# Kernel tuning notes

Measured on AMD Instinct MI355X. Metric: run time of the kernel, lower is better.

The kernel has to match this reference:

```python
import jax, jax.numpy as jnp
import numpy as np

B, T, C, H = 2, 2048, 2048, 16
HD = C // H  # head_dim = 128


def setup_inputs() -> dict:
    key = jax.random.key(0)
    k1, k2, k3 = jax.random.split(key, 3)
    x = jax.random.normal(k1, (B, T, C), dtype=jnp.float32)
    # causal mask: positions with mask==0 are blocked (masked_fill(mask==0, -inf))
    mask = jnp.tril(jnp.ones((T, T), dtype=bool))[None, None]  # [1,1,T,T]
    W_qkv = jax.random.normal(k2, (C, 3 * C), dtype=jnp.float32) * (C ** -0.5)
    W_proj = jax.random.normal(k3, (C, C), dtype=jnp.float32) * (C ** -0.5)
    b_proj = jnp.zeros((C,), dtype=jnp.float32)
    return {"x": x, "mask": mask, "W_qkv": W_qkv, "W_proj": W_proj, "b_proj": b_proj}


def reference(x, mask, W_qkv, W_proj, b_proj):
    # QKV projection (Linear, bias=False)
    qkv = jnp.einsum('btc,cd->btd', x, W_qkv)            # [B,T,3C]
    qkv = qkv.reshape(B, T, 3, H, HD)
    q = qkv[:, :, 0].transpose(0, 2, 1, 3)               # [B,H,T,HD]
    k = qkv[:, :, 1].transpose(0, 2, 1, 3)
    v = qkv[:, :, 2].transpose(0, 2, 1, 3)
    # scaled dot-product attention (dropout is identity in eval)
    att = jnp.einsum('bhqd,bhkd->bhqk', q, k) / jnp.sqrt(jnp.float32(HD))
    att = jnp.where(mask, att, -jnp.inf)
    att = jax.nn.softmax(att, axis=-1)
    y = jnp.einsum('bhqk,bhkd->bhqd', att, v)            # [B,H,T,HD]
    y = y.transpose(0, 2, 1, 3).reshape(B, T, C)
    return jnp.einsum('btc,cd->btd', y, W_proj) + b_proj
```

## Files before the change

### kernel.cpp

```cpp
#include <hip/hip_runtime.h>
#include <hip/hip_bf16.h>

#define B_  2
#define T_  2048
#define C_  2048
#define H_  16
#define HD_ 128

using bf16x8 = __attribute__((ext_vector_type(8))) __bf16;
using f32x4  = __attribute__((ext_vector_type(4))) float;

__device__ __forceinline__ unsigned short f2bs(float f) {
    __hip_bfloat16 h = __float2bfloat16(f);
    return __builtin_bit_cast(unsigned short, h);
}

__device__ __forceinline__ void gload_lds16(const unsigned short* g, unsigned short* l) {
    __builtin_amdgcn_global_load_lds(
        (const __attribute__((address_space(1))) unsigned int*)g,
        (__attribute__((address_space(3))) unsigned int*)l, 16, 0, 0);
}

__global__ __launch_bounds__(256) void k_prep(const float* __restrict__ x,
                                              unsigned short* __restrict__ XB,
                                              const float* __restrict__ Wqkv,
                                              unsigned short* __restrict__ WQKVT,
                                              const float* __restrict__ Wproj,
                                              unsigned short* __restrict__ WPROJT) {
    __shared__ unsigned short t[64][65];
    int blk = blockIdx.x;
    int tid = threadIdx.x;
    if (blk < 8192) {
        int i = blk * 256 + tid;
        float4 v = reinterpret_cast<const float4*>(x)[i];
        ushort4 o;
        o.x = f2bs(v.x); o.y = f2bs(v.y); o.z = f2bs(v.z); o.w = f2bs(v.w);
        reinterpret_cast<ushort4*>(XB)[i] = o;
        return;
    }
    const float* in;
    unsigned short* out;
    int K = 2048, N, bx, by;
    if (blk < 11264) {
        in = Wqkv; out = WQKVT; N = 6144;
        bx = (blk - 8192) % 96; by = (blk - 8192) / 96;
    } else {
        in = Wproj; out = WPROJT; N = 2048;
        bx = (blk - 11264) % 32; by = (blk - 11264) / 32;
    }
    int k0 = by * 64, n0 = bx * 64;
#pragma unroll
    for (int p = 0; p < 4; ++p) {
        int idx = p * 256 + tid;
        int r = idx >> 4, c = (idx & 15) << 2;
        float4 v = *reinterpret_cast<const float4*>(in + (long)(k0 + r) * N + n0 + c);
        t[r][c] = f2bs(v.x); t[r][c + 1] = f2bs(v.y);
        t[r][c + 2] = f2bs(v.z); t[r][c + 3] = f2bs(v.w);
    }
    __syncthreads();
#pragma unroll
    for (int p = 0; p < 4; ++p) {
        int idx = p * 256 + tid;
        int r = idx >> 4, c = (idx & 15) << 2;
        ushort4 o;
        o.x = t[c][r]; o.y = t[c + 1][r]; o.z = t[c + 2][r]; o.w = t[c + 3][r];
        *reinterpret_cast<ushort4*>(out + (long)(n0 + r) * K + k0 + c) = o;
    }
}

template <int MODE>
__global__ __launch_bounds__(256, 2) void k_gemm(const unsigned short* __restrict__ A,
                                                 const unsigned short* __restrict__ Bt,
                                                 int M, int N, int K,
                                                 unsigned short* __restrict__ qkv,
                                                 float* __restrict__ out,
                                                 const float* __restrict__ bias) {
    __shared__ __align__(16) unsigned short lA[2][128 * 32];
    __shared__ __align__(16) unsigned short lB[2][128 * 32];

    int tid = threadIdx.x;
    int wave = tid >> 6, lane = tid & 63;
    int quad = lane >> 4, l16 = lane & 15;
    int wr = (wave >> 1) * 64, wc = (wave & 1) * 64;
    int m0 = blockIdx.y * 128, n0 = blockIdx.x * 128;

    int lrow = lane >> 2;
    int lcol = (lane & 3) << 3;
    const unsigned short* gA0 = A + (long)(m0 + wave * 32 + lrow) * K + lcol;
    const unsigned short* gA1 = A + (long)(m0 + wave * 32 + 16 + lrow) * K + lcol;
    const unsigned short* gB0 = Bt + (long)(n0 + wave * 32 + lrow) * K + lcol;
    const unsigned short* gB1 = Bt + (long)(n0 + wave * 32 + 16 + lrow) * K + lcol;
    int lofs0 = wave * 1024, lofs1 = wave * 1024 + 512;

    f32x4 zero = {0.f, 0.f, 0.f, 0.f};
    f32x4 acc[4][4];
#pragma unroll
    for (int i = 0; i < 4; ++i)
#pragma unroll
        for (int j = 0; j < 4; ++j) acc[i][j] = zero;

    for (int k0 = 0; k0 < K; k0 += 64) {
        __syncthreads();
#pragma unroll
        for (int h = 0; h < 2; ++h) {
            int kk = k0 + h * 32;
            gload_lds16(gA0 + kk, &lA[h][lofs0]);
            gload_lds16(gA1 + kk, &lA[h][lofs1]);
            gload_lds16(gB0 + kk, &lB[h][lofs0]);
            gload_lds16(gB1 + kk, &lB[h][lofs1]);
        }
        __syncthreads();
#pragma unroll
        for (int h = 0; h < 2; ++h) {
            bf16x8 af[4], bfr[4];
#pragma unroll
            for (int i = 0; i < 4; ++i)
                af[i] = *reinterpret_cast<const bf16x8*>(&lA[h][(wr + i * 16 + l16) * 32 + quad * 8]);
#pragma unroll
            for (int j = 0; j < 4; ++j)
                bfr[j] = *reinterpret_cast<const bf16x8*>(&lB[h][(wc + j * 16 + l16) * 32 + quad * 8]);
#pragma unroll
            for (int i = 0; i < 4; ++i)
#pragma unroll
                for (int j = 0; j < 4; ++j)
                    acc[i][j] = __builtin_amdgcn_mfma_f32_16x16x32_bf16(af[i], bfr[j], acc[i][j], 0, 0, 0);
        }
    }

#pragma unroll
    for (int i = 0; i < 4; ++i) {
#pragma unroll
        for (int j = 0; j < 4; ++j) {
#pragma unroll
            for (int r = 0; r < 4; ++r) {
                int m = m0 + wr + i * 16 + quad * 4 + r;
                int n = n0 + wc + j * 16 + l16;
                float v = acc[i][j][r];
                if (MODE == 0) {
                    int s = n >> 11, col = n & 2047;
                    int h = col >> 7, hd = col & 127;
                    int b = m >> 11, t = m & 2047;
                    long base = (long)s * (B_ * H_ * T_ * HD_);
                    if (s == 2)
                        qkv[base + ((long)(b * H_ + h) * HD_ + hd) * T_ + t] = f2bs(v);
                    else
                        qkv[base + ((long)(b * H_ + h) * T_ + t) * HD_ + hd] = f2bs(v);
                } else {
                    out[(long)m * N + n] = v + bias[n];
                }
            }
        }
    }
}

__global__ __launch_bounds__(256, 2) void k_attn(const unsigned short* __restrict__ qkv,
                                                 unsigned short* __restrict__ y) {
    __shared__ __align__(16) unsigned short lK[64 * 136];
    __shared__ __align__(16) unsigned short lVt[128 * 72];
    __shared__ __align__(16) unsigned short lP[4][2][16 * 72];

    int tid = threadIdx.x;
    int wave = tid >> 6, lane = tid & 63;
    int quad = lane >> 4, l16 = lane & 15;
    int bh = blockIdx.x;
    int ty = (int)blockIdx.y;
    int tile = (ty < 8) ? (15 - ty) : (ty - 8);
    int qb = tile * 128;

    const unsigned short* Qh = qkv + (long)bh * (T_ * HD_);
    const unsigned short* Kh = qkv + (long)(B_ * H_) * T_ * HD_ + (long)bh * (T_ * HD_);
    const unsigned short* Vt = qkv + 2L * (B_ * H_) * T_ * HD_ + (long)bh * (HD_ * T_);

    bf16x8 aQ0[4], aQ1[4];
    const int q0_abs = qb + wave * 32 + l16;
    const int q1_abs = q0_abs + 16;
#pragma unroll
    for (int kk = 0; kk < 4; ++kk) {
        aQ0[kk] = *reinterpret_cast<const bf16x8*>(Qh + (long)q0_abs * HD_ + kk * 32 + quad * 8);
        aQ1[kk] = *reinterpret_cast<const bf16x8*>(Qh + (long)q1_abs * HD_ + kk * 32 + quad * 8);
    }

    const int kR0 = tid >> 4, kC = (tid & 15) << 3;
    const int vR0 = tid >> 3, vC = (tid & 7) << 3;

    int4 kr0, kr1, kr2, kr3, vr0, vr1, vr2, vr3;
    {
        long ko = 0;
        kr0 = *reinterpret_cast<const int4*>(Kh + (ko + kR0)      * HD_ + kC);
        kr1 = *reinterpret_cast<const int4*>(Kh + (ko + kR0 + 16) * HD_ + kC);
        kr2 = *reinterpret_cast<const int4*>(Kh + (ko + kR0 + 32) * HD_ + kC);
        kr3 = *reinterpret_cast<const int4*>(Kh + (ko + kR0 + 48) * HD_ + kC);
        vr0 = *reinterpret_cast<const int4*>(Vt + (long)(vR0)      * T_ + ko + vC);
        vr1 = *reinterpret_cast<const int4*>(Vt + (long)(vR0 + 32) * T_ + ko + vC);
        vr2 = *reinterpret_cast<const int4*>(Vt + (long)(vR0 + 64) * T_ + ko + vC);
        vr3 = *reinterpret_cast<const int4*>(Vt + (long)(vR0 + 96) * T_ + ko + vC);
    }

    float m0_ = -1e30f, l0_ = 0.f, m1_ = -1e30f, l1_ = 0.f;
    f32x4 O0[8], O1[8];
    f32x4 zero = {0.f, 0.f, 0.f, 0.f};
#pragma unroll
    for (int h = 0; h < 8; ++h) { O0[h] = zero; O1[h] = zero; }

    const float scl = 0.08838834764831845f;
    const int kbend = qb + 128;
    const int qmaxw = qb + wave * 32 + 31;

    for (int kb = 0; kb < kbend; kb += 64) {
        __syncthreads();

        *reinterpret_cast<int4*>(&lK[(kR0)      * 136 + kC]) = kr0;
        *reinterpret_cast<int4*>(&lK[(kR0 + 16) * 136 + kC]) = kr1;
        *reinterpret_cast<int4*>(&lK[(kR0 + 32) * 136 + kC]) = kr2;
        *reinterpret_cast<int4*>(&lK[(kR0 + 48) * 136 + kC]) = kr3;
        *reinterpret_cast<int4*>(&lVt[(vR0)      * 72 + vC]) = vr0;
        *reinterpret_cast<int4*>(&lVt[(vR0 + 32) * 72 + vC]) = vr1;
        *reinterpret_cast<int4*>(&lVt[(vR0 + 64) * 72 + vC]) = vr2;
        *reinterpret_cast<int4*>(&lVt[(vR0 + 96) * 72 + vC]) = vr3;

        __syncthreads();

        {
            int nkb = kb + 64;
            long ko = (nkb < kbend) ? nkb : 0;
            kr0 = *reinterpret_cast<const int4*>(Kh + (ko + kR0)      * HD_ + kC);
            kr1 = *reinterpret_cast<const int4*>(Kh + (ko + kR0 + 16) * HD_ + kC);
            kr2 = *reinterpret_cast<const int4*>(Kh + (ko + kR0 + 32) * HD_ + kC);
            kr3 = *reinterpret_cast<const int4*>(Kh + (ko + kR0 + 48) * HD_ + kC);
            vr0 = *reinterpret_cast<const int4*>(Vt + (long)(vR0)      * T_ + ko + vC);
            vr1 = *reinterpret_cast<const int4*>(Vt + (long)(vR0 + 32) * T_ + ko + vC);
            vr2 = *reinterpret_cast<const int4*>(Vt + (long)(vR0 + 64) * T_ + ko + vC);
            vr3 = *reinterpret_cast<const int4*>(Vt + (long)(vR0 + 96) * T_ + ko + vC);
        }

        if (kb > qmaxw) continue;

        f32x4 s0[4], s1[4];
#pragma unroll
        for (int st = 0; st < 4; ++st) { s0[st] = zero; s1[st] = zero; }
#pragma unroll
        for (int kk = 0; kk < 4; ++kk) {
#pragma unroll
            for (int st = 0; st < 4; ++st) {
                bf16x8 kf = *reinterpret_cast<const bf16x8*>(
                    &lK[(st * 16 + l16) * 136 + kk * 32 + quad * 8]);
                s0[st] = __builtin_amdgcn_mfma_f32_16x16x32_bf16(kf, aQ0[kk], s0[st], 0, 0, 0);
                s1[st] = __builtin_amdgcn_mfma_f32_16x16x32_bf16(kf, aQ1[kk], s1[st], 0, 0, 0);
            }
        }

        {
            float xv[4][4];
            float mx = -1e30f;
#pragma unroll
            for (int st = 0; st < 4; ++st)
#pragma unroll
                for (int r = 0; r < 4; ++r) {
                    int key = kb + st * 16 + quad * 4 + r;
                    float v = (key <= q0_abs) ? s0[st][r] * scl : -1e30f;
                    xv[st][r] = v;
                    mx = fmaxf(mx, v);
                }
            mx = fmaxf(mx, __shfl_xor(mx, 16));
            mx = fmaxf(mx, __shfl_xor(mx, 32));
            float mn = fmaxf(m0_, mx);
            float al = __expf(m0_ - mn);
            float rs = 0.f;
#pragma unroll
            for (int st = 0; st < 4; ++st)
#pragma unroll
                for (int r = 0; r < 4; ++r) {
                    float e = __expf(xv[st][r] - mn);
                    xv[st][r] = e;
                    rs += e;
                }
            rs += __shfl_xor(rs, 16);
            rs += __shfl_xor(rs, 32);
            m0_ = mn;
            l0_ = l0_ * al + rs;
#pragma unroll
            for (int st = 0; st < 4; ++st) {
                ushort4 pk;
                pk.x = f2bs(xv[st][0]); pk.y = f2bs(xv[st][1]);
                pk.z = f2bs(xv[st][2]); pk.w = f2bs(xv[st][3]);
                *reinterpret_cast<ushort4*>(&lP[wave][0][l16 * 72 + st * 16 + quad * 4]) = pk;
            }
            float alr[4];
#pragma unroll
            for (int r = 0; r < 4; ++r) alr[r] = __shfl(al, quad * 4 + r);
#pragma unroll
            for (int h = 0; h < 8; ++h)
#pragma unroll
                for (int r = 0; r < 4; ++r) O0[h][r] *= alr[r];
        }
        {
            float xv[4][4];
            float mx = -1e30f;
#pragma unroll
            for (int st = 0; st < 4; ++st)
#pragma unroll
                for (int r = 0; r < 4; ++r) {
                    int key = kb + st * 16 + quad * 4 + r;
                    float v = (key <= q1_abs) ? s1[st][r] * scl : -1e30f;
                    xv[st][r] = v;
                    mx = fmaxf(mx, v);
                }
            mx = fmaxf(mx, __shfl_xor(mx, 16));
            mx = fmaxf(mx, __shfl_xor(mx, 32));
            float mn = fmaxf(m1_, mx);
            float al = __expf(m1_ - mn);
            float rs = 0.f;
#pragma unroll
            for (int st = 0; st < 4; ++st)
#pragma unroll
                for (int r = 0; r < 4; ++r) {
                    float e = __expf(xv[st][r] - mn);
                    xv[st][r] = e;
                    rs += e;
                }
            rs += __shfl_xor(rs, 16);
            rs += __shfl_xor(rs, 32);
            m1_ = mn;
            l1_ = l1_ * al + rs;
#pragma unroll
            for (int st = 0; st < 4; ++st) {
                ushort4 pk;
                pk.x = f2bs(xv[st][0]); pk.y = f2bs(xv[st][1]);
                pk.z = f2bs(xv[st][2]); pk.w = f2bs(xv[st][3]);
                *reinterpret_cast<ushort4*>(&lP[wave][1][l16 * 72 + st * 16 + quad * 4]) = pk;
            }
            float alr[4];
#pragma unroll
            for (int r = 0; r < 4; ++r) alr[r] = __shfl(al, quad * 4 + r);
#pragma unroll
            for (int h = 0; h < 8; ++h)
#pragma unroll
                for (int r = 0; r < 4; ++r) O1[h][r] *= alr[r];
        }

#pragma unroll
        for (int kc = 0; kc < 2; ++kc) {
            bf16x8 pf0 = *reinterpret_cast<const bf16x8*>(
                &lP[wave][0][l16 * 72 + kc * 32 + quad * 8]);
            bf16x8 pf1 = *reinterpret_cast<const bf16x8*>(
                &lP[wave][1][l16 * 72 + kc * 32 + quad * 8]);
#pragma unroll
            for (int h = 0; h < 8; ++h) {
                bf16x8 vf = *reinterpret_cast<const bf16x8*>(
                    &lVt[(h * 16 + l16) * 72 + kc * 32 + quad * 8]);
                O0[h] = __builtin_amdgcn_mfma_f32_16x16x32_bf16(pf0, vf, O0[h], 0, 0, 0);
                O1[h] = __builtin_amdgcn_mfma_f32_16x16x32_bf16(pf1, vf, O1[h], 0, 0, 0);
            }
        }
    }

    int b = bh >> 4, hh = bh & 15;
#pragma unroll
    for (int r = 0; r < 4; ++r) {
        int t0 = qb + wave * 32 + quad * 4 + r;
        float inv0 = 1.f / __shfl(l0_, quad * 4 + r);
#pragma unroll
        for (int h = 0; h < 8; ++h)
            y[(long)(b * T_ + t0) * C_ + hh * HD_ + h * 16 + l16] = f2bs(O0[h][r] * inv0);
        int t1 = t0 + 16;
        float inv1 = 1.f / __shfl(l1_, quad * 4 + r);
#pragma unroll
        for (int h = 0; h < 8; ++h)
            y[(long)(b * T_ + t1) * C_ + hh * HD_ + h * 16 + l16] = f2bs(O1[h][r] * inv1);
    }
}

extern "C" void kernel_launch(void* const* d_in, const int* in_sizes, int n_in,
                              void* d_out, int out_size, void* d_ws, size_t ws_size,
                              hipStream_t stream) {
    const float* x     = (const float*)d_in[0];
    const float* Wqkv  = (const float*)d_in[2];
    const float* Wproj = (const float*)d_in[3];
    const float* bproj = (const float*)d_in[4];
    float* out = (float*)d_out;

    unsigned short* XB     = (unsigned short*)d_ws;
    unsigned short* WQKVT  = XB + 8388608;
    unsigned short* WPROJT = WQKVT + 12582912;
    unsigned short* QKV    = WPROJT + 4194304;
    if (ws_size < 100663296) return;

    k_prep<<<12288, 256, 0, stream>>>(x, XB, Wqkv, WQKVT, Wproj, WPROJT);
    k_gemm<0><<<dim3(6144 / 128, 4096 / 128), 256, 0, stream>>>(XB, WQKVT, 4096, 6144, 2048,
                                                                QKV, nullptr, nullptr);
    k_attn<<<dim3(32, 16), 256, 0, stream>>>(QKV, XB);
    k_gemm<1><<<dim3(2048 / 128, 4096 / 128), 256, 0, stream>>>(XB, WPROJT, 4096, 2048, 2048,
                                                                nullptr, out, bproj);
}
```

Measured before the change: 390.5 us.

## Double-buffer GEMM K-loop with async LDS loads and skip mask on full tiles

The GEMM main loop changes from load-all-then-compute over a 64-wide K step to a double-buffered 32-wide pipeline. The next tile's global-to-LDS load is issued before computing on the current buffer, with one barrier per step. Separately, the attention kernel skips the per-element causal mask comparison on key tiles that lie fully below the diagonal for each query row group. The aim is to hide global load latency behind MFMA work and trim VALU work in softmax. The cost is more barriers per K (one per 32 instead of two per 64) and extra code size from the branches.

```diff
diff --git a/kernel.cpp b/kernel.cpp
--- a/kernel.cpp
+++ b/kernel.cpp
@@ -99,32 +99,38 @@
 #pragma unroll
         for (int j = 0; j < 4; ++j) acc[i][j] = zero;
 
-    for (int k0 = 0; k0 < K; k0 += 64) {
+    auto stage = [&](int bi, int kk) {
+        gload_lds16(gA0 + kk, &lA[bi][lofs0]);
+        gload_lds16(gA1 + kk, &lA[bi][lofs1]);
+        gload_lds16(gB0 + kk, &lB[bi][lofs0]);
+        gload_lds16(gB1 + kk, &lB[bi][lofs1]);
+    };
+    auto compute = [&](int bi) {
+        bf16x8 af[4], bfr[4];
+#pragma unroll
+        for (int i = 0; i < 4; ++i)
+            af[i] = *reinterpret_cast<const bf16x8*>(
+                &lA[bi][(wr + i * 16 + l16) * 32 + quad * 8]);
+#pragma unroll
+        for (int j = 0; j < 4; ++j)
+            bfr[j] = *reinterpret_cast<const bf16x8*>(
+                &lB[bi][(wc + j * 16 + l16) * 32 + quad * 8]);
+#pragma unroll
+        for (int i = 0; i < 4; ++i)
+#pragma unroll
+            for (int j = 0; j < 4; ++j)
+                acc[i][j] = __builtin_amdgcn_mfma_f32_16x16x32_bf16(af[i], bfr[j],
+                                                                    acc[i][j], 0, 0, 0);
+    };
+
+    const int NT = K >> 5;
+    stage(0, 0);
+    __syncthreads();
+#pragma unroll 2
+    for (int t = 0; t < NT; ++t) {
+        if (t + 1 < NT) stage((t + 1) & 1, (t + 1) << 5);
+        compute(t & 1);
         __syncthreads();
-#pragma unroll
-        for (int h = 0; h < 2; ++h) {
-            int kk = k0 + h * 32;
-            gload_lds16(gA0 + kk, &lA[h][lofs0]);
-            gload_lds16(gA1 + kk, &lA[h][lofs1]);
-            gload_lds16(gB0 + kk, &lB[h][lofs0]);
-            gload_lds16(gB1 + kk, &lB[h][lofs1]);
-        }
-        __syncthreads();
-#pragma unroll
-        for (int h = 0; h < 2; ++h) {
-            bf16x8 af[4], bfr[4];
-#pragma unroll
-            for (int i = 0; i < 4; ++i)
-                af[i] = *reinterpret_cast<const bf16x8*>(&lA[h][(wr + i * 16 + l16) * 32 + quad * 8]);
-#pragma unroll
-            for (int j = 0; j < 4; ++j)
-                bfr[j] = *reinterpret_cast<const bf16x8*>(&lB[h][(wc + j * 16 + l16) * 32 + quad * 8]);
-#pragma unroll
-            for (int i = 0; i < 4; ++i)
-#pragma unroll
-                for (int j = 0; j < 4; ++j)
-                    acc[i][j] = __builtin_amdgcn_mfma_f32_16x16x32_bf16(af[i], bfr[j], acc[i][j], 0, 0, 0);
-        }
     }
 
 #pragma unroll
@@ -235,6 +241,9 @@
 
         if (kb > qmaxw) continue;
 
+        const bool full0 = (kb + 63) <= (qb + wave * 32);
+        const bool full1 = (kb + 63) <= (qb + wave * 32 + 16);
+
         f32x4 s0[4], s1[4];
 #pragma unroll
         for (int st = 0; st < 4; ++st) { s0[st] = zero; s1[st] = zero; }
@@ -252,15 +261,26 @@
         {
             float xv[4][4];
             float mx = -1e30f;
-#pragma unroll
-            for (int st = 0; st < 4; ++st)
-#pragma unroll
-                for (int r = 0; r < 4; ++r) {
-                    int key = kb + st * 16 + quad * 4 + r;
-                    float v = (key <= q0_abs) ? s0[st][r] * scl : -1e30f;
-                    xv[st][r] = v;
-                    mx = fmaxf(mx, v);
-                }
+            if (full0) {
+#pragma unroll
+                for (int st = 0; st < 4; ++st)
+#pragma unroll
+                    for (int r = 0; r < 4; ++r) {
+                        float v = s0[st][r] * scl;
+                        xv[st][r] = v;
+                        mx = fmaxf(mx, v);
+                    }
+            } else {
+#pragma unroll
+                for (int st = 0; st < 4; ++st)
+#pragma unroll
+                    for (int r = 0; r < 4; ++r) {
+                        int key = kb + st * 16 + quad * 4 + r;
+                        float v = (key <= q0_abs) ? s0[st][r] * scl : -1e30f;
+                        xv[st][r] = v;
+                        mx = fmaxf(mx, v);
+                    }
+            }
             mx = fmaxf(mx, __shfl_xor(mx, 16));
             mx = fmaxf(mx, __shfl_xor(mx, 32));
             float mn = fmaxf(m0_, mx);
@@ -296,15 +316,26 @@
         {
             float xv[4][4];
             float mx = -1e30f;
-#pragma unroll
-            for (int st = 0; st < 4; ++st)
-#pragma unroll
-                for (int r = 0; r < 4; ++r) {
-                    int key = kb + st * 16 + quad * 4 + r;
-                    float v = (key <= q1_abs) ? s1[st][r] * scl : -1e30f;
-                    xv[st][r] = v;
-                    mx = fmaxf(mx, v);
-                }
+            if (full1) {
+#pragma unroll
+                for (int st = 0; st < 4; ++st)
+#pragma unroll
+                    for (int r = 0; r < 4; ++r) {
+                        float v = s1[st][r] * scl;
+                        xv[st][r] = v;
+                        mx = fmaxf(mx, v);
+                    }
+            } else {
+#pragma unroll
+                for (int st = 0; st < 4; ++st)
+#pragma unroll
+                    for (int r = 0; r < 4; ++r) {
+                        int key = kb + st * 16 + quad * 4 + r;
+                        float v = (key <= q1_abs) ? s1[st][r] * scl : -1e30f;
+                        xv[st][r] = v;
+                        mx = fmaxf(mx, v);
+                    }
+            }
             mx = fmaxf(mx, __shfl_xor(mx, 16));
             mx = fmaxf(mx, __shfl_xor(mx, 32));
             float mn = fmaxf(m1_, mx);
```

Result: slower. 408.9 us (+4.7%).
